# Optimization experiments

Hardware: AMD Instinct MI355X
Metric: run time of the kernel (lower is better)

Reference implementation:

```python
import jax, jax.numpy as jnp
import numpy as np

L, B, S, E, H, V = 4, 2, 1024, 1024, 16, 32000
HD = E // H          # head_size = 64
FF = 6 * E           # FeedForward expansion = 6
EPS = 1e-5


def setup_inputs() -> dict:
    key = jax.random.key(0)
    ks = jax.random.split(key, 12)
    std = jnp.float32(0.02)

    def nrm(k, shape):
        return jax.random.normal(k, shape, jnp.float32) * std

    return {
        "x":   jax.random.randint(ks[0], (B, S), 0, V),
        "emb": nrm(ks[1], (V, E)),            # token embedding table
        "pos": nrm(ks[2], (S, E)),            # position embedding table (context = S)
        "Wq":  nrm(ks[3], (L, H, E, HD)),     # per-layer, per-head q Linear (no bias)
        "Wk":  nrm(ks[4], (L, H, E, HD)),
        "Wv":  nrm(ks[5], (L, H, E, HD)),
        "Wo":  nrm(ks[6], (L, E, E)),         # MHA output projection
        "g1":  jnp.ones((L, E), jnp.float32), "b1": jnp.zeros((L, E), jnp.float32),
        "g2":  jnp.ones((L, E), jnp.float32), "b2": jnp.zeros((L, E), jnp.float32),
        "W1":  nrm(ks[7], (L, E, FF)),        # FFN up
        "W2":  nrm(ks[8], (L, FF, E)),        # FFN down
        "gf":  jnp.ones((E,), jnp.float32), "bf": jnp.zeros((E,), jnp.float32),
        "Wf":  nrm(ks[9], (E, V)),            # final LM head (no bias)
    }


def _ln(x, g, b):
    mu = jnp.mean(x, -1, keepdims=True)
    var = jnp.mean((x - mu) ** 2, -1, keepdims=True)
    return (x - mu) * jax.lax.rsqrt(var + EPS) * g + b


def _gpt(x, emb, pos, Wq, Wk, Wv, Wo, g1, b1, g2, b2, W1, W2, gf, bf, Wf):
    Bsz, Sl = x.shape
    h = emb[x] + pos[:Sl]                         # [B,S,E]
    mask = jnp.tril(jnp.ones((Sl, Sl), bool))     # causal 'trill' buffer

    def block(h, p):
        wq, wk, wv, wo, ga, ba, gb, bb, w1, w2 = p
        z = _ln(h, ga, ba)
        q = jnp.einsum('bse,hed->bhsd', z, wq)
        k = jnp.einsum('bse,hed->bhsd', z, wk)
        v = jnp.einsum('bse,hed->bhsd', z, wv)
        att = jnp.einsum('bhsd,bhtd->bhst', q, k) * (HD ** -0.5)
        att = jnp.where(mask, att, -jnp.inf)
        att = jax.nn.softmax(att, axis=-1)
        o = jnp.einsum('bhst,bhtd->bhsd', att, v)
        o = o.transpose(0, 2, 1, 3).reshape(h.shape[0], h.shape[1], E)  # concat heads
        h = h + o @ wo                                                   # residual 1
        z = _ln(h, gb, bb)
        h = h + jax.nn.gelu(z @ w1, approximate=False) @ w2              # residual 2
        return h, None

    h, _ = jax.lax.scan(block, h, (Wq, Wk, Wv, Wo, g1, b1, g2, b2, W1, W2))
    return _ln(h, gf, bf) @ Wf                    # logits [B,S,V]


def reference(x, emb, pos, Wq, Wk, Wv, Wo, g1, b1, g2, b2, W1, W2, gf, bf, Wf):
    return _gpt(x, emb, pos, Wq, Wk, Wv, Wo, g1, b1, g2, b2, W1, W2, gf, bf, Wf)
```

## Files before the change

### kernel.cpp

```cpp
#include <hip/hip_runtime.h>
#include <hip/hip_bf16.h>
#include <math.h>


typedef unsigned short ushort_t;
typedef unsigned short us8 __attribute__((ext_vector_type(8)));
typedef unsigned short us4 __attribute__((ext_vector_type(4)));
typedef __bf16 bf16x8 __attribute__((ext_vector_type(8)));
typedef float f32x4 __attribute__((ext_vector_type(4)));

#define LN_EPS 1e-5f

__device__ inline ushort_t f2bf(float f) {
    union { float f; unsigned u; } v; v.f = f;
    unsigned r = v.u + 0x7FFFu + ((v.u >> 16) & 1u);
    return (ushort_t)(r >> 16);
}

#define GLD_LDS16(gp, lp)                                                  \
    __builtin_amdgcn_global_load_lds(                                      \
        (const __attribute__((address_space(1))) unsigned int*)(gp),       \
        (__attribute__((address_space(3))) unsigned int*)(lp), 16, 0, 0)

enum { EPI_F32 = 0, EPI_BF16 = 1, EPI_ADDF32 = 2, EPI_GELU = 3, EPI_TBF16 = 4,
       EPI_ATOM = 5, EPI_QKV = 6 };

template<int EPI, int MFR>
__global__ __launch_bounds__(512)
void gemm256(const ushort_t* __restrict__ A, const ushort_t* __restrict__ B,
             void* __restrict__ Cv, int mt, int K, int lda, int ldb, int ldc,
             long bsA, long bsB)
{
    constexpr int BM   = MFR * 32;
    constexpr int BUFE = (BM + 256) * 64;
    extern __shared__ ushort_t smem[];

    const int nwg  = gridDim.x;
    const int orig = blockIdx.x;
    int wgid = orig;
    if (nwg >= 8) {
        const int q = nwg >> 3, r = nwg & 7;
        const int xcd = orig & 7, i = orig >> 3;
        wgid = (xcd < r ? xcd * (q + 1) : r * (q + 1) + (xcd - r) * q) + i;
    }
    const int m0 = (wgid % mt) * BM;
    const int n0 = (wgid / mt) * 256;

    A += (long)blockIdx.z * bsA;
    B += (long)blockIdx.z * bsB;

    const int tid  = threadIdx.x;
    const int lane = tid & 63;
    const int wid  = tid >> 6;
    const int wm   = wid >> 2, wn = wid & 3;
    const int cg   = lane >> 4, cl = lane & 15;

    const int nt = K >> 6;

    auto stage = [&](int kt) {
        ushort_t* base = smem + (kt & 1) * BUFE;
        const int k0 = kt * 64;
        #pragma unroll
        for (int p = 0; p < MFR / 2; ++p) {
            const int chunk = p * 512 + tid;
            const int row = chunk >> 3, ch = chunk & 7;
            GLD_LDS16(&A[(long)(m0 + row) * lda + k0 + ((ch ^ (row & 7)) * 8)],
                      base + chunk * 8);
        }
        #pragma unroll
        for (int p = 0; p < 4; ++p) {
            const int chunk = p * 512 + tid;
            const int row = chunk >> 3, ch = chunk & 7;
            GLD_LDS16(&B[(long)(n0 + row) * ldb + k0 + ((ch ^ (row & 7)) * 8)],
                      base + BM * 64 + chunk * 8);
        }
    };

    stage(0);
    stage(1);
    if constexpr (MFR == 8) asm volatile("s_waitcnt vmcnt(8)" ::: "memory");
    else                    asm volatile("s_waitcnt vmcnt(6)" ::: "memory");
    __builtin_amdgcn_s_barrier();

    f32x4 acc[MFR][4] = {};

    for (int t = 0; t < nt; ++t) {
        const ushort_t* Aq = smem + (t & 1) * BUFE;
        const ushort_t* Bq = Aq + BM * 64;
        if (t >= 1 && t + 1 < nt) stage(t + 1);

        bf16x8 breg[4][2];
        #pragma unroll
        for (int nf = 0; nf < 4; ++nf) {
            const int rowB = wn * 64 + nf * 16 + cl;
            #pragma unroll
            for (int kk = 0; kk < 2; ++kk)
                breg[nf][kk] = __builtin_bit_cast(bf16x8, *(const us8*)&Bq[
                    rowB * 64 + (((kk * 4 + cg) ^ (rowB & 7)) * 8)]);
        }
        __builtin_amdgcn_s_setprio(1);
        #pragma unroll
        for (int mf = 0; mf < MFR; ++mf) {
            const int rowA = wm * (MFR * 16) + mf * 16 + cl;
            bf16x8 a0 = __builtin_bit_cast(bf16x8, *(const us8*)&Aq[
                rowA * 64 + ((cg ^ (rowA & 7)) * 8)]);
            bf16x8 a1 = __builtin_bit_cast(bf16x8, *(const us8*)&Aq[
                rowA * 64 + (((4 + cg) ^ (rowA & 7)) * 8)]);
            #pragma unroll
            for (int nf = 0; nf < 4; ++nf) {
                acc[mf][nf] = __builtin_amdgcn_mfma_f32_16x16x32_bf16(
                    a0, breg[nf][0], acc[mf][nf], 0, 0, 0);
                acc[mf][nf] = __builtin_amdgcn_mfma_f32_16x16x32_bf16(
                    a1, breg[nf][1], acc[mf][nf], 0, 0, 0);
            }
        }
        __builtin_amdgcn_s_setprio(0);
        if (t + 1 < nt) {
            asm volatile("s_waitcnt vmcnt(0) lgkmcnt(0)" ::: "memory");
            __builtin_amdgcn_s_barrier();
        }
    }

    const int rb = m0 + wm * (MFR * 16) + cg * 4;
    const int cb = n0 + wn * 64 + cl;

    #pragma unroll
    for (int mf = 0; mf < MFR; ++mf) {
        #pragma unroll
        for (int nf = 0; nf < 4; ++nf) {
            const int colg = cb + nf * 16;
            if (EPI == EPI_QKV) {
                ushort_t* Q = (ushort_t*)Cv;
                if (n0 < 1024) {
                    #pragma unroll
                    for (int r = 0; r < 4; ++r)
                        Q[(long)(rb + mf * 16 + r) * 1024 + colg] = f2bf(acc[mf][nf][r]);
                } else if (n0 < 2048) {
                    #pragma unroll
                    for (int r = 0; r < 4; ++r)
                        Q[2097152 + (long)(rb + mf * 16 + r) * 1024 + (colg - 1024)] =
                            f2bf(acc[mf][nf][r]);
                } else {
                    ushort_t* Vt = Q + 4194304;
                    const int rowg = rb + mf * 16;
                    const long boff = (long)(rowg >> 10) * 1048576;
                    us4 o4;
                    #pragma unroll
                    for (int r = 0; r < 4; ++r) o4[r] = f2bf(acc[mf][nf][r]);
                    *(us4*)&Vt[boff + (long)(colg - 2048) * 1024 + (rowg & 1023)] = o4;
                }
            } else {
                #pragma unroll
                for (int r = 0; r < 4; ++r) {
                    const int  rowg = rb + mf * 16 + r;
                    const long off  = (long)rowg * ldc + colg;
                    const float val = acc[mf][nf][r];
                    if (EPI == EPI_F32) {
                        ((float*)Cv)[off] = val;
                    } else if (EPI == EPI_GELU) {
                        float g = 0.5f * val * (1.0f + erff(val * 0.70710678118654752f));
                        ((ushort_t*)Cv)[off] = f2bf(g);
                    } else if (EPI == EPI_ATOM) {
                        atomicAdd(&((float*)Cv)[off], val);
                    } else {
                        ((ushort_t*)Cv)[off] = f2bf(val);
                    }
                }
            }
        }
    }
}

template<int EPI, int MT>
__global__ __launch_bounds__(256)
void gemm128(const ushort_t* __restrict__ A, const ushort_t* __restrict__ B,
             void* __restrict__ Cv, int K, int lda, int ldb, int ldc)
{
    const int m0 = blockIdx.x * (MT * 32);
    const int n0 = blockIdx.y * 128;

    __shared__ __align__(16) ushort_t As[MT * 32][64];
    __shared__ __align__(16) ushort_t Bs[128][64];

    const int tid  = threadIdx.x;
    const int lane = tid & 63;
    const int wid  = tid >> 6;
    const int wr   = wid >> 1, wc = wid & 1;
    const int lr   = lane >> 3;
    const int lc   = (lane & 7) * 8;
    const int cg   = lane >> 4;
    const int cl   = lane & 15;

    f32x4 acc[MT][4] = {};

    for (int k0 = 0; k0 < K; k0 += 64) {
        #pragma unroll
        for (int j = 0; j < MT; ++j) {
            const int r = wid * (8 * MT) + j * 8;
            GLD_LDS16(&A[(long)(m0 + r + lr) * lda + k0 + lc], &As[r][0]);
        }
        #pragma unroll
        for (int j = 0; j < 4; ++j) {
            const int r = wid * 32 + j * 8;
            GLD_LDS16(&B[(long)(n0 + r + lr) * ldb + k0 + lc], &Bs[r][0]);
        }
        __syncthreads();
        #pragma unroll
        for (int kk = 0; kk < 2; ++kk) {
            const int krd = kk * 32 + cg * 8;
            bf16x8 af[MT], bfr[4];
            #pragma unroll
            for (int mi = 0; mi < MT; ++mi)
                af[mi] = __builtin_bit_cast(bf16x8,
                    *(const us8*)&As[wr * (MT * 16) + mi * 16 + cl][krd]);
            #pragma unroll
            for (int nj = 0; nj < 4; ++nj)
                bfr[nj] = __builtin_bit_cast(bf16x8,
                    *(const us8*)&Bs[wc * 64 + nj * 16 + cl][krd]);
            #pragma unroll
            for (int mi = 0; mi < MT; ++mi)
                #pragma unroll
                for (int nj = 0; nj < 4; ++nj)
                    acc[mi][nj] = __builtin_amdgcn_mfma_f32_16x16x32_bf16(
                        af[mi], bfr[nj], acc[mi][nj], 0, 0, 0);
        }
        __syncthreads();
    }

    const int rb = m0 + wr * (MT * 16) + cg * 4;
    const int cb = n0 + wc * 64 + cl;

    #pragma unroll
    for (int mi = 0; mi < MT; ++mi)
        #pragma unroll
        for (int nj = 0; nj < 4; ++nj)
            #pragma unroll
            for (int r = 0; r < 4; ++r) {
                const long off = (long)(rb + mi * 16 + r) * ldc + cb + nj * 16;
                const float val = acc[mi][nj][r];
                if (EPI == EPI_ADDF32)      ((float*)Cv)[off] += val;
                else if (EPI == EPI_F32)    ((float*)Cv)[off] = val;
                else                        ((ushort_t*)Cv)[off] = f2bf(val);
            }
}

__global__ __launch_bounds__(256)
void flash_attn(const ushort_t* __restrict__ qb, const ushort_t* __restrict__ kb,
                const ushort_t* __restrict__ vT, ushort_t* __restrict__ ob)
{
    const int qt = gridDim.x - 1 - blockIdx.x;
    const int hh = blockIdx.y;
    const int bb = blockIdx.z;
    const int lane = threadIdx.x & 63;
    const int w    = threadIdx.x >> 6;
    const int cg   = lane >> 4;
    const int cl   = lane & 15;

    __shared__ __align__(16) ushort_t P_lds[4][16][72];

    const int q0 = qt * 64;
    const long tokQ = (long)bb * 1024 + q0 + w * 16 + cl;

    bf16x8 qf[2];
    #pragma unroll
    for (int kk = 0; kk < 2; ++kk)
        qf[kk] = __builtin_bit_cast(bf16x8,
            *(const us8*)&qb[tokQ * 1024 + hh * 64 + kk * 32 + cg * 8]);

    const ushort_t* kbase = kb + (long)bb * 1048576 + hh * 64;
    const ushort_t* vbase = vT + (long)bb * 1048576 + (long)hh * 65536;

    f32x4 o[4] = {};
    float m4[4], l4[4];
    #pragma unroll
    for (int r = 0; r < 4; ++r) { m4[r] = -1e30f; l4[r] = 0.0f; }

    for (int tt = 0; tt <= qt; ++tt) {
        const int t0 = tt * 64;
        f32x4 s[4] = {};
        __builtin_amdgcn_s_setprio(1);
        #pragma unroll
        for (int nj = 0; nj < 4; ++nj) {
            const ushort_t* kp = kbase + (long)(t0 + nj * 16 + cl) * 1024 + cg * 8;
            bf16x8 kf0 = __builtin_bit_cast(bf16x8, *(const us8*)kp);
            bf16x8 kf1 = __builtin_bit_cast(bf16x8, *(const us8*)(kp + 32));
            s[nj] = __builtin_amdgcn_mfma_f32_16x16x32_bf16(qf[0], kf0, s[nj], 0, 0, 0);
            s[nj] = __builtin_amdgcn_mfma_f32_16x16x32_bf16(qf[1], kf1, s[nj], 0, 0, 0);
        }
        __builtin_amdgcn_s_setprio(0);
        const bool diag = (tt == qt);
        float pm[4] = {-3e30f, -3e30f, -3e30f, -3e30f};
        #pragma unroll
        for (int nj = 0; nj < 4; ++nj)
            #pragma unroll
            for (int r = 0; r < 4; ++r) {
                float v = s[nj][r] * 0.125f;
                if (diag && (t0 + nj * 16 + cl) > (q0 + w * 16 + cg * 4 + r))
                    v = -1e30f;
                s[nj][r] = v;
                pm[r] = fmaxf(pm[r], v);
            }
        #pragma unroll
        for (int r = 0; r < 4; ++r)
            #pragma unroll
            for (int msk = 1; msk < 16; msk <<= 1)
                pm[r] = fmaxf(pm[r], __shfl_xor(pm[r], msk));
        float al[4], ps[4];
        #pragma unroll
        for (int r = 0; r < 4; ++r) {
            const float mn = fmaxf(m4[r], pm[r]);
            al[r] = __expf(m4[r] - mn);
            m4[r] = mn;
            ps[r] = 0.0f;
        }
        #pragma unroll
        for (int nj = 0; nj < 4; ++nj)
            #pragma unroll
            for (int r = 0; r < 4; ++r) {
                const float p = __expf(s[nj][r] - m4[r]);
                s[nj][r] = p;
                ps[r] += p;
            }
        #pragma unroll
        for (int r = 0; r < 4; ++r) {
            #pragma unroll
            for (int msk = 1; msk < 16; msk <<= 1)
                ps[r] += __shfl_xor(ps[r], msk);
            l4[r] = l4[r] * al[r] + ps[r];
        }
        #pragma unroll
        for (int nj = 0; nj < 4; ++nj)
            #pragma unroll
            for (int r = 0; r < 4; ++r) o[nj][r] *= al[r];
        #pragma unroll
        for (int nj = 0; nj < 4; ++nj)
            #pragma unroll
            for (int r = 0; r < 4; ++r)
                P_lds[w][cg * 4 + r][nj * 16 + cl] = f2bf(s[nj][r]);
        asm volatile("s_waitcnt lgkmcnt(0)" ::: "memory");
        __builtin_amdgcn_sched_barrier(0);
        bf16x8 pa[2];
        #pragma unroll
        for (int kk = 0; kk < 2; ++kk)
            pa[kk] = __builtin_bit_cast(bf16x8,
                *(const us8*)&P_lds[w][cl][kk * 32 + cg * 8]);
        __builtin_amdgcn_s_setprio(1);
        #pragma unroll
        for (int nj = 0; nj < 4; ++nj) {
            const ushort_t* vp = vbase + (long)(nj * 16 + cl) * 1024 + t0 + cg * 8;
            bf16x8 vf0 = __builtin_bit_cast(bf16x8, *(const us8*)vp);
            bf16x8 vf1 = __builtin_bit_cast(bf16x8, *(const us8*)(vp + 32));
            o[nj] = __builtin_amdgcn_mfma_f32_16x16x32_bf16(pa[0], vf0, o[nj], 0, 0, 0);
            o[nj] = __builtin_amdgcn_mfma_f32_16x16x32_bf16(pa[1], vf1, o[nj], 0, 0, 0);
        }
        __builtin_amdgcn_s_setprio(0);
    }

    #pragma unroll
    for (int r = 0; r < 4; ++r) {
        const float inv = 1.0f / l4[r];
        const long tok = (long)bb * 1024 + q0 + w * 16 + cg * 4 + r;
        #pragma unroll
        for (int nj = 0; nj < 4; ++nj)
            ob[tok * 1024 + hh * 64 + nj * 16 + cl] = f2bf(o[nj][r] * inv);
    }
}

__global__ __launch_bounds__(256)
void transpose_conv(const float* __restrict__ in, ushort_t* __restrict__ out,
                    long ldin, long ldout, long bsin, long bsout,
                    long bsout_hi, int zmod)
{
    __shared__ float tile[32][33];
    const int tx = threadIdx.x, ty = threadIdx.y;
    const long bin  = (long)blockIdx.z * bsin;
    const long bout = (long)(blockIdx.z % zmod) * bsout
                    + (long)(blockIdx.z / zmod) * bsout_hi;
    const int n0 = blockIdx.x * 32, k0 = blockIdx.y * 32;
    #pragma unroll
    for (int i = 0; i < 4; ++i)
        tile[ty + i * 8][tx] = in[bin + (long)(k0 + ty + i * 8) * ldin + n0 + tx];
    __syncthreads();
    #pragma unroll
    for (int i = 0; i < 4; ++i) {
        const int n = ty + i * 8;
        out[bout + (long)(n0 + n) * ldout + k0 + tx] = f2bf(tile[tx][n]);
    }
}

__global__ __launch_bounds__(256)
void embed_kernel(const int* __restrict__ x, const float* __restrict__ emb,
                  const float* __restrict__ pos, float* __restrict__ h)
{
    const int row = blockIdx.x, tid = threadIdx.x;
    const int s = row & 1023;
    const int idx = x[row];
    const float4 e = ((const float4*)(emb + (long)idx * 1024))[tid];
    const float4 p = ((const float4*)(pos + (long)s * 1024))[tid];
    float4 o; o.x = e.x + p.x; o.y = e.y + p.y; o.z = e.z + p.z; o.w = e.w + p.w;
    ((float4*)(h + (long)row * 1024))[tid] = o;
}

__global__ __launch_bounds__(256)
void ln_kernel(const float* __restrict__ x, const float* __restrict__ g,
               const float* __restrict__ b, ushort_t* __restrict__ z)
{
    const int row = blockIdx.x, tid = threadIdx.x;
    const float4 v = ((const float4*)(x + (long)row * 1024))[tid];
    float s  = v.x + v.y + v.z + v.w;
    float sq = v.x * v.x + v.y * v.y + v.z * v.z + v.w * v.w;
    #pragma unroll
    for (int o = 32; o > 0; o >>= 1) { s += __shfl_down(s, o); sq += __shfl_down(sq, o); }
    __shared__ float ls[4], lq[4];
    if ((tid & 63) == 0) { ls[tid >> 6] = s; lq[tid >> 6] = sq; }
    __syncthreads();
    s  = ls[0] + ls[1] + ls[2] + ls[3];
    sq = lq[0] + lq[1] + lq[2] + lq[3];
    const float mu   = s * (1.0f / 1024.0f);
    const float var  = sq * (1.0f / 1024.0f) - mu * mu;
    const float rstd = rsqrtf(var + LN_EPS);
    const float4 gg = ((const float4*)g)[tid];
    const float4 bb = ((const float4*)b)[tid];
    us4 o4;
    o4[0] = f2bf((v.x - mu) * rstd * gg.x + bb.x);
    o4[1] = f2bf((v.y - mu) * rstd * gg.y + bb.y);
    o4[2] = f2bf((v.z - mu) * rstd * gg.z + bb.z);
    o4[3] = f2bf((v.w - mu) * rstd * gg.w + bb.w);
    *(us4*)(z + (long)row * 1024 + tid * 4) = o4;
}

extern "C" void kernel_launch(void* const* d_in, const int* in_sizes, int n_in,
                              void* d_out, int out_size, void* d_ws, size_t ws_size,
                              hipStream_t stream)
{
    const int*   x   = (const int*)  d_in[0];
    const float* emb = (const float*)d_in[1];
    const float* pos = (const float*)d_in[2];
    const float* Wq  = (const float*)d_in[3];
    const float* Wk  = (const float*)d_in[4];
    const float* Wv  = (const float*)d_in[5];
    const float* Wo  = (const float*)d_in[6];
    const float* g1  = (const float*)d_in[7];
    const float* b1  = (const float*)d_in[8];
    const float* g2  = (const float*)d_in[9];
    const float* b2  = (const float*)d_in[10];
    const float* W1  = (const float*)d_in[11];
    const float* W2  = (const float*)d_in[12];
    const float* gf  = (const float*)d_in[13];
    const float* bfp = (const float*)d_in[14];
    const float* Wf  = (const float*)d_in[15];
    float* out = (float*)d_out;

    char* ws = (char*)d_ws;
    size_t off = 0;
    auto alloc = [&](size_t bytes) {
        char* p = ws + off;
        off = (off + bytes + 255) & ~(size_t)255;
        return p;
    };
    ushort_t* WqkvT = (ushort_t*)alloc(4UL * 3145728 * 2);
    ushort_t* WoT   = (ushort_t*)alloc(4UL * 1048576 * 2);
    ushort_t* W1T   = (ushort_t*)alloc(4UL * 6291456 * 2);
    ushort_t* W2T   = (ushort_t*)alloc(4UL * 6291456 * 2);
    ushort_t* WfT   = (ushort_t*)alloc(32768000UL * 2);
    float*    h     = (float*)   alloc(2048UL * 1024 * 4);
    ushort_t* z     = (ushort_t*)alloc(2048UL * 1024 * 2);
    ushort_t* qb    = (ushort_t*)alloc(3UL * 2048 * 1024 * 2);
    ushort_t* kb    = qb + 2097152;
    ushort_t* vT    = qb + 4194304;
    ushort_t* ob    = (ushort_t*)alloc(2048UL * 1024 * 2);
    ushort_t* ub    = (ushort_t*)alloc(2048UL * 6144 * 2);
    (void)ws_size; (void)in_sizes; (void)n_in; (void)out_size;

    const int LDS8 = 2 * (256 + 256) * 64 * 2;
    const int LDS4 = 2 * (128 + 256) * 64 * 2;
    hipFuncSetAttribute((const void*)&gemm256<EPI_F32, 8>,
                        hipFuncAttributeMaxDynamicSharedMemorySize, LDS8);
    hipFuncSetAttribute((const void*)&gemm256<EPI_GELU, 8>,
                        hipFuncAttributeMaxDynamicSharedMemorySize, LDS8);
    hipFuncSetAttribute((const void*)&gemm256<EPI_ATOM, 8>,
                        hipFuncAttributeMaxDynamicSharedMemorySize, LDS8);
    hipFuncSetAttribute((const void*)&gemm256<EPI_QKV, 4>,
                        hipFuncAttributeMaxDynamicSharedMemorySize, LDS4);

    const dim3 tb(32, 8);
    transpose_conv<<<dim3(2,   32, 64), tb, 0, stream>>>(Wq, WqkvT,           64, 1024, 65536, 65536, 3145728, 16);
    transpose_conv<<<dim3(2,   32, 64), tb, 0, stream>>>(Wk, WqkvT + 1048576, 64, 1024, 65536, 65536, 3145728, 16);
    transpose_conv<<<dim3(2,   32, 64), tb, 0, stream>>>(Wv, WqkvT + 2097152, 64, 1024, 65536, 65536, 3145728, 16);
    transpose_conv<<<dim3(32,  32,  4), tb, 0, stream>>>(Wo, WoT, 1024,  1024, 1048576, 1048576, 0, 4);
    transpose_conv<<<dim3(192, 32,  4), tb, 0, stream>>>(W1, W1T, 6144,  1024, 6291456, 6291456, 0, 4);
    transpose_conv<<<dim3(32, 192,  4), tb, 0, stream>>>(W2, W2T, 1024,  6144, 6291456, 6291456, 0, 4);
    transpose_conv<<<dim3(1000,32,  1), tb, 0, stream>>>(Wf, WfT, 32000, 1024, 0,       0,       0, 1);

    embed_kernel<<<2048, 256, 0, stream>>>(x, emb, pos, h);

    for (int l = 0; l < 4; ++l) {
        const size_t wff = (size_t)l * 6291456;

        ln_kernel<<<2048, 256, 0, stream>>>(h, g1 + l * 1024, b1 + l * 1024, z);

        gemm256<EPI_QKV, 4><<<dim3(16 * 12), 512, LDS4, stream>>>(
            z, WqkvT + (size_t)l * 3145728, qb, 16, 1024, 1024, 1024, 0, 0, 0);

        flash_attn<<<dim3(16, 16, 2), 256, 0, stream>>>(qb, kb, vT, ob);

        gemm128<EPI_ADDF32, 2><<<dim3(32, 8), 256, 0, stream>>>(
            ob, WoT + (size_t)l * 1048576, h, 1024, 1024, 1024, 1024);

        ln_kernel<<<2048, 256, 0, stream>>>(h, g2 + l * 1024, b2 + l * 1024, z);

        gemm256<EPI_GELU, 8><<<dim3(8 * 24), 512, LDS8, stream>>>(
            z, W1T + wff, ub, 8, 1024, 1024, 1024, 6144, 0, 0);
        gemm256<EPI_ATOM, 8><<<dim3(8 * 4, 1, 8), 512, LDS8, stream>>>(
            ub, W2T + wff, h, 8, 768, 6144, 6144, 1024, 768, 768);
    }

    ln_kernel<<<2048, 256, 0, stream>>>(h, gf, bfp, z);
    gemm256<EPI_F32, 8><<<dim3(8 * 125), 512, LDS8, stream>>>(
        z, WfT, out, 8, 1024, 1024, 1024, 32000, 0, 0);
}
```

Measured before the change: 1.267 ms.

## Switch GEMM to four-stage K=32 LDS pipeline with prefetch depth three

Replaces the double-buffered K=64 tile pipeline in the shared GEMM kernel with four LDS buffers of K=32 each. Global-to-LDS loads run three stages ahead. Graded vmcnt waits let each barrier wait only for the next stage instead of draining all outstanding loads. Total LDS use stays the same, but the swizzle changes for 32-wide rows and there are twice as many barriers per K with half the MFMA work between them.

```diff
diff --git a/kernel.cpp b/kernel.cpp
--- a/kernel.cpp
+++ b/kernel.cpp
@@ -27,12 +27,12 @@
 
 template<int EPI, int MFR>
 __global__ __launch_bounds__(512)
-void gemm256(const ushort_t* __restrict__ A, const ushort_t* __restrict__ B,
-             void* __restrict__ Cv, int mt, int K, int lda, int ldb, int ldc,
-             long bsA, long bsB)
+void gemmP(const ushort_t* __restrict__ A, const ushort_t* __restrict__ B,
+           void* __restrict__ Cv, int mt, int K, int lda, int ldb, int ldc,
+           long bsA, long bsB)
 {
     constexpr int BM   = MFR * 32;
-    constexpr int BUFE = (BM + 256) * 64;
+    constexpr int BUFE = (BM + 256) * 32;
     extern __shared__ ushort_t smem[];
 
     const int nwg  = gridDim.x;
@@ -55,29 +55,31 @@
     const int wm   = wid >> 2, wn = wid & 3;
     const int cg   = lane >> 4, cl = lane & 15;
 
-    const int nt = K >> 6;
+    const int nt = K >> 5;
 
     auto stage = [&](int kt) {
-        ushort_t* base = smem + (kt & 1) * BUFE;
-        const int k0 = kt * 64;
-        #pragma unroll
-        for (int p = 0; p < MFR / 2; ++p) {
+        ushort_t* base = smem + (kt & 3) * BUFE;
+        const int k0 = kt * 32;
+        #pragma unroll
+        for (int p = 0; p < MFR / 4; ++p) {
             const int chunk = p * 512 + tid;
-            const int row = chunk >> 3, ch = chunk & 7;
-            GLD_LDS16(&A[(long)(m0 + row) * lda + k0 + ((ch ^ (row & 7)) * 8)],
-                      base + chunk * 8);
-        }
-        #pragma unroll
-        for (int p = 0; p < 4; ++p) {
+            const int row = chunk >> 2, pc = chunk & 3;
+            const int lc  = (pc ^ ((row >> 1) & 3)) * 8;
+            GLD_LDS16(&A[(long)(m0 + row) * lda + k0 + lc], base + chunk * 8);
+        }
+        #pragma unroll
+        for (int p = 0; p < 2; ++p) {
             const int chunk = p * 512 + tid;
-            const int row = chunk >> 3, ch = chunk & 7;
-            GLD_LDS16(&B[(long)(n0 + row) * ldb + k0 + ((ch ^ (row & 7)) * 8)],
-                      base + BM * 64 + chunk * 8);
+            const int row = chunk >> 2, pc = chunk & 3;
+            const int lc  = (pc ^ ((row >> 1) & 3)) * 8;
+            GLD_LDS16(&B[(long)(n0 + row) * ldb + k0 + lc],
+                      base + BM * 32 + chunk * 8);
         }
     };
 
     stage(0);
     stage(1);
+    stage(2);
     if constexpr (MFR == 8) asm volatile("s_waitcnt vmcnt(8)" ::: "memory");
     else                    asm volatile("s_waitcnt vmcnt(6)" ::: "memory");
     __builtin_amdgcn_s_barrier();
@@ -85,38 +87,46 @@
     f32x4 acc[MFR][4] = {};
 
     for (int t = 0; t < nt; ++t) {
-        const ushort_t* Aq = smem + (t & 1) * BUFE;
-        const ushort_t* Bq = Aq + BM * 64;
-        if (t >= 1 && t + 1 < nt) stage(t + 1);
-
-        bf16x8 breg[4][2];
+        const ushort_t* Aq = smem + (t & 3) * BUFE;
+        const ushort_t* Bq = Aq + BM * 32;
+        if (t + 3 < nt) stage(t + 3);
+
+        bf16x8 breg[4];
         #pragma unroll
         for (int nf = 0; nf < 4; ++nf) {
             const int rowB = wn * 64 + nf * 16 + cl;
-            #pragma unroll
-            for (int kk = 0; kk < 2; ++kk)
-                breg[nf][kk] = __builtin_bit_cast(bf16x8, *(const us8*)&Bq[
-                    rowB * 64 + (((kk * 4 + cg) ^ (rowB & 7)) * 8)]);
+            breg[nf] = __builtin_bit_cast(bf16x8, *(const us8*)&Bq[
+                rowB * 32 + ((cg ^ ((rowB >> 1) & 3)) * 8)]);
         }
         __builtin_amdgcn_s_setprio(1);
         #pragma unroll
         for (int mf = 0; mf < MFR; ++mf) {
             const int rowA = wm * (MFR * 16) + mf * 16 + cl;
-            bf16x8 a0 = __builtin_bit_cast(bf16x8, *(const us8*)&Aq[
-                rowA * 64 + ((cg ^ (rowA & 7)) * 8)]);
-            bf16x8 a1 = __builtin_bit_cast(bf16x8, *(const us8*)&Aq[
-                rowA * 64 + (((4 + cg) ^ (rowA & 7)) * 8)]);
-            #pragma unroll
-            for (int nf = 0; nf < 4; ++nf) {
+            bf16x8 a = __builtin_bit_cast(bf16x8, *(const us8*)&Aq[
+                rowA * 32 + ((cg ^ ((rowA >> 1) & 3)) * 8)]);
+            #pragma unroll
+            for (int nf = 0; nf < 4; ++nf)
                 acc[mf][nf] = __builtin_amdgcn_mfma_f32_16x16x32_bf16(
-                    a0, breg[nf][0], acc[mf][nf], 0, 0, 0);
-                acc[mf][nf] = __builtin_amdgcn_mfma_f32_16x16x32_bf16(
-                    a1, breg[nf][1], acc[mf][nf], 0, 0, 0);
+                    a, breg[nf], acc[mf][nf], 0, 0, 0);
+        }
+        __builtin_amdgcn_s_setprio(0);
+
+        if (t + 1 < nt) {
+            if constexpr (MFR == 8) {
+                if (t + 3 < nt)
+                    asm volatile("s_waitcnt vmcnt(8) lgkmcnt(0)" ::: "memory");
+                else if (t + 2 < nt)
+                    asm volatile("s_waitcnt vmcnt(4) lgkmcnt(0)" ::: "memory");
+                else
+                    asm volatile("s_waitcnt vmcnt(0) lgkmcnt(0)" ::: "memory");
+            } else {
+                if (t + 3 < nt)
+                    asm volatile("s_waitcnt vmcnt(6) lgkmcnt(0)" ::: "memory");
+                else if (t + 2 < nt)
+                    asm volatile("s_waitcnt vmcnt(3) lgkmcnt(0)" ::: "memory");
+                else
+                    asm volatile("s_waitcnt vmcnt(0) lgkmcnt(0)" ::: "memory");
             }
-        }
-        __builtin_amdgcn_s_setprio(0);
-        if (t + 1 < nt) {
-            asm volatile("s_waitcnt vmcnt(0) lgkmcnt(0)" ::: "memory");
             __builtin_amdgcn_s_barrier();
         }
     }
@@ -472,15 +482,15 @@
     ushort_t* ub    = (ushort_t*)alloc(2048UL * 6144 * 2);
     (void)ws_size; (void)in_sizes; (void)n_in; (void)out_size;
 
-    const int LDS8 = 2 * (256 + 256) * 64 * 2;
-    const int LDS4 = 2 * (128 + 256) * 64 * 2;
-    hipFuncSetAttribute((const void*)&gemm256<EPI_F32, 8>,
+    const int LDS8 = 4 * (256 + 256) * 32 * 2;
+    const int LDS4 = 4 * (128 + 256) * 32 * 2;
+    hipFuncSetAttribute((const void*)&gemmP<EPI_F32, 8>,
                         hipFuncAttributeMaxDynamicSharedMemorySize, LDS8);
-    hipFuncSetAttribute((const void*)&gemm256<EPI_GELU, 8>,
+    hipFuncSetAttribute((const void*)&gemmP<EPI_GELU, 8>,
                         hipFuncAttributeMaxDynamicSharedMemorySize, LDS8);
-    hipFuncSetAttribute((const void*)&gemm256<EPI_ATOM, 8>,
+    hipFuncSetAttribute((const void*)&gemmP<EPI_ATOM, 8>,
                         hipFuncAttributeMaxDynamicSharedMemorySize, LDS8);
-    hipFuncSetAttribute((const void*)&gemm256<EPI_QKV, 4>,
+    hipFuncSetAttribute((const void*)&gemmP<EPI_QKV, 4>,
                         hipFuncAttributeMaxDynamicSharedMemorySize, LDS4);
 
     const dim3 tb(32, 8);
@@ -499,7 +509,7 @@
 
         ln_kernel<<<2048, 256, 0, stream>>>(h, g1 + l * 1024, b1 + l * 1024, z);
 
-        gemm256<EPI_QKV, 4><<<dim3(16 * 12), 512, LDS4, stream>>>(
+        gemmP<EPI_QKV, 4><<<dim3(16 * 12), 512, LDS4, stream>>>(
             z, WqkvT + (size_t)l * 3145728, qb, 16, 1024, 1024, 1024, 0, 0, 0);
 
         flash_attn<<<dim3(16, 16, 2), 256, 0, stream>>>(qb, kb, vT, ob);
@@ -509,13 +519,13 @@
 
         ln_kernel<<<2048, 256, 0, stream>>>(h, g2 + l * 1024, b2 + l * 1024, z);
 
-        gemm256<EPI_GELU, 8><<<dim3(8 * 24), 512, LDS8, stream>>>(
+        gemmP<EPI_GELU, 8><<<dim3(8 * 24), 512, LDS8, stream>>>(
             z, W1T + wff, ub, 8, 1024, 1024, 1024, 6144, 0, 0);
-        gemm256<EPI_ATOM, 8><<<dim3(8 * 4, 1, 8), 512, LDS8, stream>>>(
+        gemmP<EPI_ATOM, 8><<<dim3(8 * 4, 1, 8), 512, LDS8, stream>>>(
             ub, W2T + wff, h, 8, 768, 6144, 6144, 1024, 768, 768);
     }
 
     ln_kernel<<<2048, 256, 0, stream>>>(h, gf, bfp, z);
-    gemm256<EPI_F32, 8><<<dim3(8 * 125), 512, LDS8, stream>>>(
+    gemmP<EPI_F32, 8><<<dim3(8 * 125), 512, LDS8, stream>>>(
         z, WfT, out, 8, 1024, 1024, 1024, 32000, 0, 0);
 }
```

Result: slower. 1.312 ms (+3.6%).

## Replace GEMM with 256x128 tile, triple-buffered LDS pipeline

Applied to the files above, without the earlier changes.

The templated 256x256 / 128x256 GEMM is replaced by a single 256x128 tiled kernel whose LDS holds three stages, so global-to-LDS loads run two K-steps ahead and wait on a partial vmcnt instead of draining all loads each iteration. Grid sizes for the QKV, FFN-up, FFN-down (split-K reduced from 8 to 4) and LM-head GEMMs are adjusted to match. This aims for deeper latency hiding and more workgroups per GEMM. In exchange each tile does fewer MFMAs per loaded byte, and the vmcnt(6) count has to match the number of loads issued per stage.

```diff
diff --git a/kernel.cpp b/kernel.cpp
--- a/kernel.cpp
+++ b/kernel.cpp
@@ -25,14 +25,13 @@
 enum { EPI_F32 = 0, EPI_BF16 = 1, EPI_ADDF32 = 2, EPI_GELU = 3, EPI_TBF16 = 4,
        EPI_ATOM = 5, EPI_QKV = 6 };
 
-template<int EPI, int MFR>
+template<int EPI>
 __global__ __launch_bounds__(512)
-void gemm256(const ushort_t* __restrict__ A, const ushort_t* __restrict__ B,
-             void* __restrict__ Cv, int mt, int K, int lda, int ldb, int ldc,
-             long bsA, long bsB)
-{
-    constexpr int BM   = MFR * 32;
-    constexpr int BUFE = (BM + 256) * 64;
+void gemmT(const ushort_t* __restrict__ A, const ushort_t* __restrict__ B,
+           void* __restrict__ Cv, int mt, int K, int lda, int ldb, int ldc,
+           long bsA, long bsB)
+{
+    constexpr int BUFE = (256 + 128) * 64;
     extern __shared__ ushort_t smem[];
 
     const int nwg  = gridDim.x;
@@ -43,8 +42,8 @@
         const int xcd = orig & 7, i = orig >> 3;
         wgid = (xcd < r ? xcd * (q + 1) : r * (q + 1) + (xcd - r) * q) + i;
     }
-    const int m0 = (wgid % mt) * BM;
-    const int n0 = (wgid / mt) * 256;
+    const int m0 = (wgid % mt) * 256;
+    const int n0 = (wgid / mt) * 128;
 
     A += (long)blockIdx.z * bsA;
     B += (long)blockIdx.z * bsB;
@@ -52,42 +51,42 @@
     const int tid  = threadIdx.x;
     const int lane = tid & 63;
     const int wid  = tid >> 6;
-    const int wm   = wid >> 2, wn = wid & 3;
+    const int wm   = wid >> 1, wn = wid & 1;
     const int cg   = lane >> 4, cl = lane & 15;
 
     const int nt = K >> 6;
 
     auto stage = [&](int kt) {
-        ushort_t* base = smem + (kt & 1) * BUFE;
+        ushort_t* base = smem + (kt % 3) * BUFE;
         const int k0 = kt * 64;
-        #pragma unroll
-        for (int p = 0; p < MFR / 2; ++p) {
-            const int chunk = p * 512 + tid;
-            const int row = chunk >> 3, ch = chunk & 7;
-            GLD_LDS16(&A[(long)(m0 + row) * lda + k0 + ((ch ^ (row & 7)) * 8)],
-                      base + chunk * 8);
-        }
         #pragma unroll
         for (int p = 0; p < 4; ++p) {
             const int chunk = p * 512 + tid;
-            const int row = chunk >> 3, ch = chunk & 7;
-            GLD_LDS16(&B[(long)(n0 + row) * ldb + k0 + ((ch ^ (row & 7)) * 8)],
-                      base + BM * 64 + chunk * 8);
+            const int row = chunk >> 3, pc = chunk & 7;
+            const int lc  = (pc ^ (row & 7)) * 8;
+            GLD_LDS16(&A[(long)(m0 + row) * lda + k0 + lc], base + chunk * 8);
+        }
+        #pragma unroll
+        for (int p = 0; p < 2; ++p) {
+            const int chunk = p * 512 + tid;
+            const int row = chunk >> 3, pc = chunk & 7;
+            const int lc  = (pc ^ (row & 7)) * 8;
+            GLD_LDS16(&B[(long)(n0 + row) * ldb + k0 + lc],
+                      base + 16384 + chunk * 8);
         }
     };
 
     stage(0);
     stage(1);
-    if constexpr (MFR == 8) asm volatile("s_waitcnt vmcnt(8)" ::: "memory");
-    else                    asm volatile("s_waitcnt vmcnt(6)" ::: "memory");
+    asm volatile("s_waitcnt vmcnt(6)" ::: "memory");
     __builtin_amdgcn_s_barrier();
 
-    f32x4 acc[MFR][4] = {};
+    f32x4 acc[4][4] = {};
 
     for (int t = 0; t < nt; ++t) {
-        const ushort_t* Aq = smem + (t & 1) * BUFE;
-        const ushort_t* Bq = Aq + BM * 64;
-        if (t >= 1 && t + 1 < nt) stage(t + 1);
+        const ushort_t* Aq = smem + (t % 3) * BUFE;
+        const ushort_t* Bq = Aq + 16384;
+        if (t + 2 < nt) stage(t + 2);
 
         bf16x8 breg[4][2];
         #pragma unroll
@@ -100,8 +99,8 @@
         }
         __builtin_amdgcn_s_setprio(1);
         #pragma unroll
-        for (int mf = 0; mf < MFR; ++mf) {
-            const int rowA = wm * (MFR * 16) + mf * 16 + cl;
+        for (int mf = 0; mf < 4; ++mf) {
+            const int rowA = wm * 64 + mf * 16 + cl;
             bf16x8 a0 = __builtin_bit_cast(bf16x8, *(const us8*)&Aq[
                 rowA * 64 + ((cg ^ (rowA & 7)) * 8)]);
             bf16x8 a1 = __builtin_bit_cast(bf16x8, *(const us8*)&Aq[
@@ -115,17 +114,21 @@
             }
         }
         __builtin_amdgcn_s_setprio(0);
+
         if (t + 1 < nt) {
-            asm volatile("s_waitcnt vmcnt(0) lgkmcnt(0)" ::: "memory");
+            if (t + 2 < nt)
+                asm volatile("s_waitcnt vmcnt(6) lgkmcnt(0)" ::: "memory");
+            else
+                asm volatile("s_waitcnt vmcnt(0) lgkmcnt(0)" ::: "memory");
             __builtin_amdgcn_s_barrier();
         }
     }
 
-    const int rb = m0 + wm * (MFR * 16) + cg * 4;
+    const int rb = m0 + wm * 64 + cg * 4;
     const int cb = n0 + wn * 64 + cl;
 
     #pragma unroll
-    for (int mf = 0; mf < MFR; ++mf) {
+    for (int mf = 0; mf < 4; ++mf) {
         #pragma unroll
         for (int nf = 0; nf < 4; ++nf) {
             const int colg = cb + nf * 16;
@@ -472,16 +475,15 @@
     ushort_t* ub    = (ushort_t*)alloc(2048UL * 6144 * 2);
     (void)ws_size; (void)in_sizes; (void)n_in; (void)out_size;
 
-    const int LDS8 = 2 * (256 + 256) * 64 * 2;
-    const int LDS4 = 2 * (128 + 256) * 64 * 2;
-    hipFuncSetAttribute((const void*)&gemm256<EPI_F32, 8>,
-                        hipFuncAttributeMaxDynamicSharedMemorySize, LDS8);
-    hipFuncSetAttribute((const void*)&gemm256<EPI_GELU, 8>,
-                        hipFuncAttributeMaxDynamicSharedMemorySize, LDS8);
-    hipFuncSetAttribute((const void*)&gemm256<EPI_ATOM, 8>,
-                        hipFuncAttributeMaxDynamicSharedMemorySize, LDS8);
-    hipFuncSetAttribute((const void*)&gemm256<EPI_QKV, 4>,
-                        hipFuncAttributeMaxDynamicSharedMemorySize, LDS4);
+    const int LDST = 3 * 24576 * 2;
+    hipFuncSetAttribute((const void*)&gemmT<EPI_F32>,
+                        hipFuncAttributeMaxDynamicSharedMemorySize, LDST);
+    hipFuncSetAttribute((const void*)&gemmT<EPI_GELU>,
+                        hipFuncAttributeMaxDynamicSharedMemorySize, LDST);
+    hipFuncSetAttribute((const void*)&gemmT<EPI_ATOM>,
+                        hipFuncAttributeMaxDynamicSharedMemorySize, LDST);
+    hipFuncSetAttribute((const void*)&gemmT<EPI_QKV>,
+                        hipFuncAttributeMaxDynamicSharedMemorySize, LDST);
 
     const dim3 tb(32, 8);
     transpose_conv<<<dim3(2,   32, 64), tb, 0, stream>>>(Wq, WqkvT,           64, 1024, 65536, 65536, 3145728, 16);
@@ -499,8 +501,8 @@
 
         ln_kernel<<<2048, 256, 0, stream>>>(h, g1 + l * 1024, b1 + l * 1024, z);
 
-        gemm256<EPI_QKV, 4><<<dim3(16 * 12), 512, LDS4, stream>>>(
-            z, WqkvT + (size_t)l * 3145728, qb, 16, 1024, 1024, 1024, 0, 0, 0);
+        gemmT<EPI_QKV><<<dim3(8 * 24), 512, LDST, stream>>>(
+            z, WqkvT + (size_t)l * 3145728, qb, 8, 1024, 1024, 1024, 1024, 0, 0);
 
         flash_attn<<<dim3(16, 16, 2), 256, 0, stream>>>(qb, kb, vT, ob);
 
@@ -509,13 +511,13 @@
 
         ln_kernel<<<2048, 256, 0, stream>>>(h, g2 + l * 1024, b2 + l * 1024, z);
 
-        gemm256<EPI_GELU, 8><<<dim3(8 * 24), 512, LDS8, stream>>>(
+        gemmT<EPI_GELU><<<dim3(8 * 48), 512, LDST, stream>>>(
             z, W1T + wff, ub, 8, 1024, 1024, 1024, 6144, 0, 0);
-        gemm256<EPI_ATOM, 8><<<dim3(8 * 4, 1, 8), 512, LDS8, stream>>>(
-            ub, W2T + wff, h, 8, 768, 6144, 6144, 1024, 768, 768);
+        gemmT<EPI_ATOM><<<dim3(8 * 8, 1, 4), 512, LDST, stream>>>(
+            ub, W2T + wff, h, 8, 1536, 6144, 6144, 1024, 1536, 1536);
     }
 
     ln_kernel<<<2048, 256, 0, stream>>>(h, gf, bfp, z);
-    gemm256<EPI_F32, 8><<<dim3(8 * 125), 512, LDS8, stream>>>(
+    gemmT<EPI_F32><<<dim3(8 * 250), 512, LDST, stream>>>(
         z, WfT, out, 8, 1024, 1024, 1024, 32000, 0, 0);
 }
```

New measurement: 1.230 ms. 2.9% less time.
